# Kernel tuning notes

Measured on AMD Instinct MI355X. Metric: run time of the kernel, lower is better.

The kernel has to match this reference:

```python
import jax, jax.numpy as jnp
import numpy as np

T = 16384      # total packed tokens
C = 1024       # d_model
H = 16         # n_head
HD = C // H    # head dim = 64
N_SEG = 32     # number of equal varlen segments
SEG = T // N_SEG


def setup_inputs() -> dict:
    key = jax.random.key(0)
    k1, k2, k3 = jax.random.split(key, 3)
    x = jax.random.normal(k1, (T, C), dtype=jnp.float32)
    w_attn = jax.random.normal(k2, (C, 3 * C), dtype=jnp.float32) * (1.0 / np.sqrt(C))
    w_proj = jax.random.normal(k3, (C, C), dtype=jnp.float32) * (1.0 / np.sqrt(C))
    # boundary indices for torch.tensor_split -> 32 equal segments of SEG tokens
    split_sections = (jnp.arange(1, N_SEG) * SEG).astype(jnp.int64)
    return {"x": x, "w_attn": w_attn, "w_proj": w_proj, "split_sections": split_sections}


def reference(x, w_attn, w_proj, split_sections):
    # x: [T, C] packed tokens; split_sections: 31 boundaries -> 32 equal segments
    n_seg = int(np.asarray(split_sections).shape[0]) + 1
    seg = x.shape[0] // n_seg
    qkv = x @ w_attn                                   # [T, 3C]
    q, k, v = jnp.split(qkv, 3, axis=-1)               # each [T, C]

    def heads(t):
        # [T, C] -> [H, n_seg, seg, HD]  (block-diagonal segment layout)
        return t.reshape(x.shape[0], H, HD).transpose(1, 0, 2).reshape(H, n_seg, seg, HD)

    q, k, v = heads(q), heads(k), heads(v)
    scale = 1.0 / np.sqrt(HD)
    att = jnp.einsum('hnqd,hnkd->hnqk', q, k) * scale  # [H, n_seg, seg, seg]
    att = jax.nn.softmax(att, axis=-1)
    y = jnp.einsum('hnqk,hnkd->hnqd', att, v)          # [H, n_seg, seg, HD]
    y = y.reshape(H, x.shape[0], HD).transpose(1, 0, 2).reshape(x.shape[0], C)
    return y @ w_proj                                  # [T, C]
```

## Files before the change

kernel.cpp:

```cpp
#include <hip/hip_runtime.h>
#include <hip/hip_bf16.h>
#include <stdint.h>

typedef __attribute__((ext_vector_type(8))) short short8;
typedef __attribute__((ext_vector_type(4))) short short4_t;
typedef __attribute__((ext_vector_type(4))) float float4_t;

#define GLOAD_LDS16(gp, lp)                                                              \
  __builtin_amdgcn_global_load_lds((const __attribute__((address_space(1))) unsigned int*)(gp), \
                                   (__attribute__((address_space(3))) unsigned int*)(lp), \
                                   16, 0, 0)

__device__ __forceinline__ float4_t mfma_bf16(short8 a, short8 b, float4_t c) {
  return __builtin_amdgcn_mfma_f32_16x16x32_bf16(a, b, c, 0, 0, 0);
}

__device__ __forceinline__ short f2bf(float f) {
  union { float f; unsigned int u; } v; v.f = f;
  unsigned int r = v.u + 0x7fff + ((v.u >> 16) & 1);
  return (short)(r >> 16);
}

__device__ __forceinline__ float red_sum16(float v) {
  v += __shfl_xor(v, 1);
  v += __shfl_xor(v, 2);
  v += __shfl_xor(v, 4);
  v += __shfl_xor(v, 8);
  return v;
}

__device__ __forceinline__ long swz_col(long colbase64, int chunk, int sub, int row) {
  return colbase64 + ((chunk ^ (row & 7)) << 3) + sub;
}

__global__ __launch_bounds__(256) void conv_swz(const float* __restrict__ in,
                                                short* __restrict__ out, long nchunks) {
  for (long ch = (long)blockIdx.x * blockDim.x + threadIdx.x; ch < nchunks;
       ch += (long)gridDim.x * blockDim.x) {
    long r  = ch >> 7;
    int cir = (int)(ch & 127);
    int pc  = (cir & ~7) | ((cir & 7) ^ ((int)r & 7));
    const float* src = in + ch * 8;
    short8 o;
#pragma unroll
    for (int j = 0; j < 8; ++j) o[j] = f2bf(src[j]);
    *(short8*)&out[r * 1024 + pc * 8] = o;
  }
}

__global__ __launch_bounds__(256) void transpose_conv(const float* __restrict__ in,
                                                      short* __restrict__ out,
                                                      int R, int C) {
  __shared__ short tile[32][33];
  int c0 = blockIdx.x * 32;
  int r0 = blockIdx.y * 32;
  int tx = threadIdx.x;
  int ty = threadIdx.y;
#pragma unroll
  for (int i = 0; i < 4; ++i)
    tile[ty + i * 8][tx] = f2bf(in[(long)(r0 + ty + i * 8) * C + c0 + tx]);
  __syncthreads();
#pragma unroll
  for (int i = 0; i < 4; ++i) {
    int n   = c0 + ty + i * 8;
    int col = r0 + tx;
    long cc = swz_col((long)(col & ~63), (col >> 3) & 7, col & 7, n);
    out[(long)n * R + cc] = tile[tx][ty + i * 8];
  }
}

template <int MODE>
__global__ __launch_bounds__(256, 2) void gemm_bt(const short* __restrict__ A, long lda,
                                                  const short* __restrict__ Bt,
                                                  void* __restrict__ Cv,
                                                  short* __restrict__ vT,
                                                  int M, int N, int K) {
  __shared__ __align__(16) short As[128 * 64];
  __shared__ __align__(16) short Bs[128 * 64];

  const int tid  = threadIdx.x;
  const int wave = tid >> 6;
  const int lane = tid & 63;
  const int rA   = lane & 15;
  const int q4   = lane >> 4;
  const long m0  = (long)blockIdx.y * 128;
  const long n0  = (long)blockIdx.x * 128;
  const int wm   = (wave & 1) * 64;
  const int wn   = (wave >> 1) * 64;

  float4_t acc[4][4];
#pragma unroll
  for (int i = 0; i < 4; ++i)
#pragma unroll
    for (int j = 0; j < 4; ++j) acc[i][j] = (float4_t){0.f, 0.f, 0.f, 0.f};

  for (int k0 = 0; k0 < K; k0 += 64) {
#pragma unroll
    for (int i = 0; i < 4; ++i) {
      int slot = i * 256 + tid;
      int r    = slot >> 3;
      int c    = slot & 7;
      const short* ga = A  + (m0 + r) * lda      + k0 + c * 8;
      const short* gb = Bt + (n0 + r) * (long)K  + k0 + c * 8;
      GLOAD_LDS16(ga, &As[(i * 256 + wave * 64) * 8]);
      GLOAD_LDS16(gb, &Bs[(i * 256 + wave * 64) * 8]);
    }
    __syncthreads();
#pragma unroll
    for (int kk = 0; kk < 2; ++kk) {
      int cp = (kk * 4 + q4) ^ (rA & 7);
      short8 af[4], bfr[4];
#pragma unroll
      for (int mi = 0; mi < 4; ++mi) {
        int r  = wm + mi * 16 + rA;
        af[mi] = *(const short8*)&As[(r * 8 + cp) * 8];
      }
#pragma unroll
      for (int ni = 0; ni < 4; ++ni) {
        int r  = wn + ni * 16 + rA;
        bfr[ni] = *(const short8*)&Bs[(r * 8 + cp) * 8];
      }
#pragma unroll
      for (int mi = 0; mi < 4; ++mi)
#pragma unroll
        for (int ni = 0; ni < 4; ++ni)
          acc[mi][ni] = mfma_bf16(af[mi], bfr[ni], acc[mi][ni]);
    }
    __syncthreads();
  }

  if constexpr (MODE == 1) {
    short* Cq = (short*)Cv;
    if (n0 >= 2048) {
#pragma unroll
      for (int mi = 0; mi < 4; ++mi) {
        int tbase = (int)m0 + wm + mi * 16 + q4 * 4;
        int ct    = (tbase >> 3) & 7;
#pragma unroll
        for (int ni = 0; ni < 4; ++ni) {
          int c = (int)n0 + wn + ni * 16 + rA;
          int d = c - 2048;
          long dst = (long)d * 16384 + (long)(tbase & ~63) +
                     (((ct ^ (d & 7))) << 3) + (tbase & 7);
          short4_t o;
#pragma unroll
          for (int reg = 0; reg < 4; ++reg) o[reg] = f2bf(acc[mi][ni][reg]);
          *(short4_t*)&vT[dst] = o;
        }
      }
    } else {
#pragma unroll
      for (int mi = 0; mi < 4; ++mi)
#pragma unroll
        for (int ni = 0; ni < 4; ++ni)
#pragma unroll
          for (int reg = 0; reg < 4; ++reg) {
            long t = m0 + wm + mi * 16 + q4 * 4 + reg;
            int  c = (int)n0 + wn + ni * 16 + rA;
            long cc = swz_col((long)(c & ~63), (c >> 3) & 7, c & 7, (int)t);
            Cq[t * 3072 + cc] = f2bf(acc[mi][ni][reg]);
          }
    }
  } else {
    float* Co = (float*)Cv;
#pragma unroll
    for (int mi = 0; mi < 4; ++mi)
#pragma unroll
      for (int ni = 0; ni < 4; ++ni)
#pragma unroll
        for (int reg = 0; reg < 4; ++reg) {
          long row = m0 + wm + mi * 16 + q4 * 4 + reg;
          long col = n0 + wn + ni * 16 + rA;
          Co[row * (long)N + col] = acc[mi][ni][reg];
        }
  }
}

__global__ __launch_bounds__(256, 2) void attn_kernel(short* __restrict__ qkv,
                                                      const short* __restrict__ vT) {
  __shared__ __align__(16) short Qs[128 * 64];
  __shared__ __align__(16) short Ks[2][64 * 64];
  __shared__ __align__(16) short Vt[2][64 * 64];
  __shared__ __align__(16) short Ps[128 * 72];

  const int tid  = threadIdx.x;
  const int wave = tid >> 6;
  const int lane = tid & 63;
  const int rA   = lane & 15;
  const int q4   = lane >> 4;
  const int qt   = blockIdx.x;
  const int seg  = blockIdx.y;
  const int h    = blockIdx.z;

  const long tq0  = (long)seg * 512 + qt * 128;
  const long tk0  = (long)seg * 512;
  const long hoff = (long)h * 64;

#pragma unroll
  for (int i = 0; i < 4; ++i) {
    int slot = i * 256 + tid;
    int r    = slot >> 3;
    int c    = slot & 7;
    GLOAD_LDS16(qkv + (tq0 + r) * 3072 + hoff + c * 8, &Qs[(i * 256 + wave * 64) * 8]);
  }
#pragma unroll
  for (int i = 0; i < 2; ++i) {
    int slot = i * 256 + tid;
    int r    = slot >> 3;
    int c    = slot & 7;
    GLOAD_LDS16(qkv + (tk0 + r) * 3072 + 1024 + hoff + c * 8,
                &Ks[0][(i * 256 + wave * 64) * 8]);
    GLOAD_LDS16(vT + (hoff + r) * 16384 + tk0 + c * 8,
                &Vt[0][(i * 256 + wave * 64) * 8]);
  }

  float4_t acc_o[2][4];
  float l_st[2][4];
#pragma unroll
  for (int mi = 0; mi < 2; ++mi)
#pragma unroll
    for (int di = 0; di < 4; ++di) acc_o[mi][di] = (float4_t){0.f, 0.f, 0.f, 0.f};
#pragma unroll
  for (int mi = 0; mi < 2; ++mi)
#pragma unroll
    for (int reg = 0; reg < 4; ++reg) l_st[mi][reg] = 0.f;

  for (int kt = 0; kt < 8; ++kt) {
    const int p = kt & 1;
    __syncthreads();

    if (kt < 7) {
      const long tkn = tk0 + (kt + 1) * 64;
#pragma unroll
      for (int i = 0; i < 2; ++i) {
        int slot = i * 256 + tid;
        int r    = slot >> 3;
        int c    = slot & 7;
        GLOAD_LDS16(qkv + (tkn + r) * 3072 + 1024 + hoff + c * 8,
                    &Ks[1 - p][(i * 256 + wave * 64) * 8]);
        GLOAD_LDS16(vT + (hoff + r) * 16384 + tkn + c * 8,
                    &Vt[1 - p][(i * 256 + wave * 64) * 8]);
      }
    }

    float4_t s_acc[2][4];
#pragma unroll
    for (int mi = 0; mi < 2; ++mi)
#pragma unroll
      for (int ni = 0; ni < 4; ++ni) s_acc[mi][ni] = (float4_t){0.f, 0.f, 0.f, 0.f};
#pragma unroll
    for (int kk = 0; kk < 2; ++kk) {
      int cp = (kk * 4 + q4) ^ (rA & 7);
      short8 af[2], bfr[4];
#pragma unroll
      for (int mi = 0; mi < 2; ++mi) {
        int r  = wave * 32 + mi * 16 + rA;
        af[mi] = *(const short8*)&Qs[(r * 8 + cp) * 8];
      }
#pragma unroll
      for (int ni = 0; ni < 4; ++ni) {
        int r  = ni * 16 + rA;
        bfr[ni] = *(const short8*)&Ks[p][(r * 8 + cp) * 8];
      }
#pragma unroll
      for (int mi = 0; mi < 2; ++mi)
#pragma unroll
        for (int ni = 0; ni < 4; ++ni)
          s_acc[mi][ni] = mfma_bf16(af[mi], bfr[ni], s_acc[mi][ni]);
    }

#pragma unroll
    for (int mi = 0; mi < 2; ++mi)
#pragma unroll
      for (int reg = 0; reg < 4; ++reg) {
        float rs = 0.f;
#pragma unroll
        for (int ni = 0; ni < 4; ++ni) {
          float pv = __expf(s_acc[mi][ni][reg] * 0.125f);
          s_acc[mi][ni][reg] = pv;
          rs += pv;
        }
        l_st[mi][reg] += rs;
      }

#pragma unroll
    for (int mi = 0; mi < 2; ++mi)
#pragma unroll
      for (int ni = 0; ni < 4; ++ni)
#pragma unroll
        for (int reg = 0; reg < 4; ++reg)
          Ps[(wave * 32 + mi * 16 + q4 * 4 + reg) * 72 + ni * 16 + rA] =
              f2bf(s_acc[mi][ni][reg]);

    __syncthreads();

#pragma unroll
    for (int kk = 0; kk < 2; ++kk) {
      int cp = (kk * 4 + q4) ^ (rA & 7);
      short8 af[2], bfr[4];
#pragma unroll
      for (int mi = 0; mi < 2; ++mi)
        af[mi] = *(const short8*)&Ps[(wave * 32 + mi * 16 + rA) * 72 + (kk * 4 + q4) * 8];
#pragma unroll
      for (int di = 0; di < 4; ++di)
        bfr[di] = *(const short8*)&Vt[p][((di * 16 + rA) * 8 + cp) * 8];
#pragma unroll
      for (int mi = 0; mi < 2; ++mi)
#pragma unroll
        for (int di = 0; di < 4; ++di)
          acc_o[mi][di] = mfma_bf16(af[mi], bfr[di], acc_o[mi][di]);
    }
  }

#pragma unroll
  for (int mi = 0; mi < 2; ++mi)
#pragma unroll
    for (int reg = 0; reg < 4; ++reg) {
      float l  = red_sum16(l_st[mi][reg]);
      float rl = 1.0f / l;
      long t = tq0 + wave * 32 + mi * 16 + q4 * 4 + reg;
#pragma unroll
      for (int di = 0; di < 4; ++di) {
        int c  = di * 16 + rA;
        long cc = hoff + (((c >> 3) ^ ((int)t & 7)) << 3) + (c & 7);
        qkv[t * 3072 + cc] = f2bf(acc_o[mi][di][reg] * rl);
      }
    }
}

extern "C" void kernel_launch(void* const* d_in, const int* in_sizes, int n_in,
                              void* d_out, int out_size, void* d_ws, size_t ws_size,
                              hipStream_t stream) {
  const float* x      = (const float*)d_in[0];
  const float* w_attn = (const float*)d_in[1];
  const float* w_proj = (const float*)d_in[2];
  float* out = (float*)d_out;

  short* wT_a = (short*)d_ws;
  short* wT_p = wT_a + (size_t)3072 * 1024;
  short* qkv  = wT_p + (size_t)1024 * 1024;

  short* xb = (short*)d_out;
  short* vT = xb + (size_t)16384 * 1024;

  conv_swz<<<2048, 256, 0, stream>>>(x, xb, (long)16384 * 1024 / 8);
  transpose_conv<<<dim3(3072 / 32, 1024 / 32), dim3(32, 8), 0, stream>>>(w_attn, wT_a, 1024, 3072);
  transpose_conv<<<dim3(1024 / 32, 1024 / 32), dim3(32, 8), 0, stream>>>(w_proj, wT_p, 1024, 1024);

  gemm_bt<1><<<dim3(3072 / 128, 16384 / 128), 256, 0, stream>>>(xb, 1024, wT_a, qkv, vT, 16384, 3072, 1024);

  attn_kernel<<<dim3(4, 32, 16), 256, 0, stream>>>(qkv, vT);

  gemm_bt<2><<<dim3(1024 / 128, 16384 / 128), 256, 0, stream>>>(qkv, 3072, wT_p, out, nullptr, 16384, 1024, 1024);
}
```

Measured before the change: 355.9 us.

## Replace 128x128 GEMM with 256x256 multi-stage pipelined GEMM and 4-way swizzle

Result: slower. 367.5 us (+3.3%).

```diff
diff --git a/kernel.cpp b/kernel.cpp
--- a/kernel.cpp
+++ b/kernel.cpp
@@ -39,7 +39,7 @@
        ch += (long)gridDim.x * blockDim.x) {
     long r  = ch >> 7;
     int cir = (int)(ch & 127);
-    int pc  = (cir & ~7) | ((cir & 7) ^ ((int)r & 7));
+    int pc  = (cir & ~3) | ((cir & 3) ^ ((int)r & 3));
     const float* src = in + ch * 8;
     short8 o;
 #pragma unroll
@@ -63,84 +63,122 @@
 #pragma unroll
   for (int i = 0; i < 4; ++i) {
     int n   = c0 + ty + i * 8;
-    int col = r0 + tx;
-    long cc = swz_col((long)(col & ~63), (col >> 3) & 7, col & 7, n);
+    long cc = (long)r0 + (((tx >> 3) ^ (n & 3)) << 3) + (tx & 7);
     out[(long)n * R + cc] = tile[tx][ty + i * 8];
   }
 }
 
 template <int MODE>
-__global__ __launch_bounds__(256, 2) void gemm_bt(const short* __restrict__ A, long lda,
-                                                  const short* __restrict__ Bt,
+__global__ __launch_bounds__(512, 2) void gemm256(const short* __restrict__ A, long lda,
+                                                  const short* __restrict__ Bt, long ldb,
                                                   void* __restrict__ Cv,
                                                   short* __restrict__ vT,
                                                   int M, int N, int K) {
-  __shared__ __align__(16) short As[128 * 64];
-  __shared__ __align__(16) short Bs[128 * 64];
+  __shared__ __align__(16) short As[4][256 * 32];
+  __shared__ __align__(16) short Bs[4][256 * 32];
 
   const int tid  = threadIdx.x;
   const int wave = tid >> 6;
   const int lane = tid & 63;
   const int rA   = lane & 15;
   const int q4   = lane >> 4;
-  const long m0  = (long)blockIdx.y * 128;
-  const long n0  = (long)blockIdx.x * 128;
-  const int wm   = (wave & 1) * 64;
-  const int wn   = (wave >> 1) * 64;
-
-  float4_t acc[4][4];
-#pragma unroll
-  for (int i = 0; i < 4; ++i)
+  const int wm   = (wave >> 2) * 128;
+  const int wn   = (wave & 3) * 64;
+
+  const int nbx = N >> 8;
+  const int nwg = nbx * (M >> 8);
+  const int bid = (int)blockIdx.y * nbx + (int)blockIdx.x;
+  const int cpx = nwg >> 3;
+  const int swz = (bid & 7) * cpx + (bid >> 3);
+  const long m0 = (long)(swz / nbx) * 256;
+  const long n0 = (long)(swz % nbx) * 256;
+
+  const short* Ag = A  + (m0 + (tid >> 2)) * lda + (tid & 3) * 8;
+  const short* Bg = Bt + (n0 + (tid >> 2)) * ldb + (tid & 3) * 8;
+
+#define STAGE_A(u)                                                          \
+  {                                                                         \
+    const int slot_ = (u) & 3;                                              \
+    GLOAD_LDS16(Ag + (u) * 32,             &As[slot_][wave * 512]);         \
+    GLOAD_LDS16(Ag + 128 * lda + (u) * 32, &As[slot_][4096 + wave * 512]);  \
+  }
+#define STAGE_B(u)                                                          \
+  {                                                                         \
+    const int slot_ = (u) & 3;                                              \
+    GLOAD_LDS16(Bg + (u) * 32,             &Bs[slot_][wave * 512]);         \
+    GLOAD_LDS16(Bg + 128 * ldb + (u) * 32, &Bs[slot_][4096 + wave * 512]);  \
+  }
+
+  float4_t acc[8][4];
+#pragma unroll
+  for (int i = 0; i < 8; ++i)
 #pragma unroll
     for (int j = 0; j < 4; ++j) acc[i][j] = (float4_t){0.f, 0.f, 0.f, 0.f};
 
-  for (int k0 = 0; k0 < K; k0 += 64) {
-#pragma unroll
-    for (int i = 0; i < 4; ++i) {
-      int slot = i * 256 + tid;
-      int r    = slot >> 3;
-      int c    = slot & 7;
-      const short* ga = A  + (m0 + r) * lda      + k0 + c * 8;
-      const short* gb = Bt + (n0 + r) * (long)K  + k0 + c * 8;
-      GLOAD_LDS16(ga, &As[(i * 256 + wave * 64) * 8]);
-      GLOAD_LDS16(gb, &Bs[(i * 256 + wave * 64) * 8]);
-    }
-    __syncthreads();
-#pragma unroll
-    for (int kk = 0; kk < 2; ++kk) {
-      int cp = (kk * 4 + q4) ^ (rA & 7);
-      short8 af[4], bfr[4];
-#pragma unroll
-      for (int mi = 0; mi < 4; ++mi) {
-        int r  = wm + mi * 16 + rA;
-        af[mi] = *(const short8*)&As[(r * 8 + cp) * 8];
-      }
-#pragma unroll
-      for (int ni = 0; ni < 4; ++ni) {
-        int r  = wn + ni * 16 + rA;
-        bfr[ni] = *(const short8*)&Bs[(r * 8 + cp) * 8];
-      }
-#pragma unroll
-      for (int mi = 0; mi < 4; ++mi)
-#pragma unroll
-        for (int ni = 0; ni < 4; ++ni)
-          acc[mi][ni] = mfma_bf16(af[mi], bfr[ni], acc[mi][ni]);
-    }
-    __syncthreads();
-  }
+  const int nt = K >> 5;
+
+  STAGE_A(0); STAGE_B(0);
+  STAGE_A(1); STAGE_B(1);
+  STAGE_A(2); STAGE_B(2);
+  asm volatile("s_waitcnt vmcnt(4)" ::: "memory");
+  __builtin_amdgcn_s_barrier();
+
+  const int cswz = q4 ^ (rA & 3);
+
+  for (int u = 0; u < nt; ++u) {
+    const int slot = u & 3;
+    short8 af[4], bfr[4];
+#pragma unroll
+    for (int mi = 0; mi < 4; ++mi)
+      af[mi] = *(const short8*)&As[slot][((wm + mi * 16 + rA) * 4 + cswz) * 8];
+#pragma unroll
+    for (int ni = 0; ni < 4; ++ni)
+      bfr[ni] = *(const short8*)&Bs[slot][((wn + ni * 16 + rA) * 4 + cswz) * 8];
+    if (u + 3 < nt) STAGE_A(u + 3);
+    __builtin_amdgcn_s_barrier();
+    __builtin_amdgcn_s_setprio(1);
+#pragma unroll
+    for (int mi = 0; mi < 4; ++mi)
+#pragma unroll
+      for (int ni = 0; ni < 4; ++ni)
+        acc[mi][ni] = mfma_bf16(af[mi], bfr[ni], acc[mi][ni]);
+    __builtin_amdgcn_s_setprio(0);
+    __builtin_amdgcn_s_barrier();
+#pragma unroll
+    for (int mi = 0; mi < 4; ++mi)
+      af[mi] = *(const short8*)&As[slot][((wm + 64 + mi * 16 + rA) * 4 + cswz) * 8];
+    if (u + 3 < nt) STAGE_B(u + 3);
+    __builtin_amdgcn_s_barrier();
+    __builtin_amdgcn_s_setprio(1);
+#pragma unroll
+    for (int mi = 0; mi < 4; ++mi)
+#pragma unroll
+      for (int ni = 0; ni < 4; ++ni)
+        acc[mi + 4][ni] = mfma_bf16(af[mi], bfr[ni], acc[mi + 4][ni]);
+    __builtin_amdgcn_s_setprio(0);
+    {
+      const int rem = nt - 2 - u;
+      if (rem >= 2)      asm volatile("s_waitcnt vmcnt(8)" ::: "memory");
+      else if (rem == 1) asm volatile("s_waitcnt vmcnt(4)" ::: "memory");
+      else               asm volatile("s_waitcnt vmcnt(0)" ::: "memory");
+    }
+    __builtin_amdgcn_s_barrier();
+  }
+#undef STAGE_A
+#undef STAGE_B
 
   if constexpr (MODE == 1) {
     short* Cq = (short*)Cv;
     if (n0 >= 2048) {
 #pragma unroll
-      for (int mi = 0; mi < 4; ++mi) {
+      for (int mi = 0; mi < 8; ++mi) {
         int tbase = (int)m0 + wm + mi * 16 + q4 * 4;
         int ct    = (tbase >> 3) & 7;
 #pragma unroll
         for (int ni = 0; ni < 4; ++ni) {
           int c = (int)n0 + wn + ni * 16 + rA;
           int d = c - 2048;
-          long dst = (long)d * 16384 + (long)(tbase & ~63) +
+          long dst = (long)d * 16384 + (tbase & ~63) +
                      (((ct ^ (d & 7))) << 3) + (tbase & 7);
           short4_t o;
 #pragma unroll
@@ -150,7 +188,7 @@
       }
     } else {
 #pragma unroll
-      for (int mi = 0; mi < 4; ++mi)
+      for (int mi = 0; mi < 8; ++mi)
 #pragma unroll
         for (int ni = 0; ni < 4; ++ni)
 #pragma unroll
@@ -163,8 +201,9 @@
     }
   } else {
     float* Co = (float*)Cv;
-#pragma unroll
-    for (int mi = 0; mi < 4; ++mi)
+    (void)vT;
+#pragma unroll
+    for (int mi = 0; mi < 8; ++mi)
 #pragma unroll
       for (int ni = 0; ni < 4; ++ni)
 #pragma unroll
@@ -322,7 +361,7 @@
 #pragma unroll
       for (int di = 0; di < 4; ++di) {
         int c  = di * 16 + rA;
-        long cc = hoff + (((c >> 3) ^ ((int)t & 7)) << 3) + (c & 7);
+        long cc = hoff + (c & 32) + ((((c >> 3) & 3) ^ ((int)t & 3)) << 3) + (c & 7);
         qkv[t * 3072 + cc] = f2bf(acc_o[mi][di][reg] * rl);
       }
     }
@@ -347,9 +386,11 @@
   transpose_conv<<<dim3(3072 / 32, 1024 / 32), dim3(32, 8), 0, stream>>>(w_attn, wT_a, 1024, 3072);
   transpose_conv<<<dim3(1024 / 32, 1024 / 32), dim3(32, 8), 0, stream>>>(w_proj, wT_p, 1024, 1024);
 
-  gemm_bt<1><<<dim3(3072 / 128, 16384 / 128), 256, 0, stream>>>(xb, 1024, wT_a, qkv, vT, 16384, 3072, 1024);
+  gemm256<1><<<dim3(3072 / 256, 16384 / 256), 512, 0, stream>>>(xb, 1024, wT_a, 1024, qkv, vT,
+                                                                16384, 3072, 1024);
 
   attn_kernel<<<dim3(4, 32, 16), 256, 0, stream>>>(qkv, vT);
 
-  gemm_bt<2><<<dim3(1024 / 128, 16384 / 128), 256, 0, stream>>>(qkv, 3072, wT_p, out, nullptr, 16384, 1024, 1024);
-}
+  gemm256<2><<<dim3(1024 / 256, 16384 / 256), 512, 0, stream>>>(qkv, 3072, wT_p, 1024, out, nullptr,
+                                                                16384, 1024, 1024);
+}
```
